# Kernel tuning notes

Hardware: AMD Instinct MI355X
Metric: run time of the kernel (lower is better)

## Reference

```python
import jax, jax.numpy as jnp
import numpy as np

EPS = 1e-6
NUM_HEADS = 16


def _layer_norm(x):
    # LayerNorm32: fp32 layernorm, eps=1e-6, no affine params
    m = jnp.mean(x, axis=-1, keepdims=True)
    v = jnp.var(x, axis=-1, keepdims=True)
    return (x - m) * jax.lax.rsqrt(v + EPS)


def setup_inputs() -> dict:
    key = jax.random.key(0)
    ks = jax.random.split(key, 6)
    B, L, C = 4, 2048, 1024
    H = 4 * C
    s = 0.02
    return {
        "x": jax.random.normal(ks[0], (B, L, C), dtype=jnp.float32),
        "qkv_w": jax.random.normal(ks[1], (C, 3 * C), dtype=jnp.float32) * s,
        "qkv_b": jnp.zeros((3 * C,), dtype=jnp.float32),
        "proj_w": jax.random.normal(ks[2], (C, C), dtype=jnp.float32) * s,
        "proj_b": jnp.zeros((C,), dtype=jnp.float32),
        "fc1_w": jax.random.normal(ks[3], (C, H), dtype=jnp.float32) * s,
        "fc1_b": jnp.zeros((H,), dtype=jnp.float32),
        "fc2_w": jax.random.normal(ks[4], (H, C), dtype=jnp.float32) * s,
        "fc2_b": jnp.zeros((C,), dtype=jnp.float32),
    }


def _block(x, qkv_w, qkv_b, proj_w, proj_b, fc1_w, fc1_b, fc2_w, fc2_b):
    B, L, C = x.shape
    Hn = NUM_HEADS
    D = C // Hn

    # --- attention branch (pre-norm) ---
    h = _layer_norm(x)
    qkv = h @ qkv_w + qkv_b                      # [B, L, 3C]
    qkv = qkv.reshape(B, L, 3, Hn, D)
    q, k, v = qkv[:, :, 0], qkv[:, :, 1], qkv[:, :, 2]  # [B, L, Hn, D]
    scale = 1.0 / jnp.sqrt(jnp.asarray(D, dtype=x.dtype))
    logits = jnp.einsum("bqhd,bkhd->bhqk", q, k) * scale
    attn = jax.nn.softmax(logits, axis=-1)
    o = jnp.einsum("bhqk,bkhd->bqhd", attn, v).reshape(B, L, C)
    o = o @ proj_w + proj_b
    x = x + o

    # --- MLP branch (pre-norm) ---
    h = _layer_norm(x)
    h = jax.nn.gelu(h @ fc1_w + fc1_b, approximate=True)  # tanh GELU
    h = h @ fc2_w + fc2_b
    return x + h


def reference(x, qkv_w, qkv_b, proj_w, proj_b, fc1_w, fc1_b, fc2_w, fc2_b):
    return _block(x, qkv_w, qkv_b, proj_w, proj_b, fc1_w, fc1_b, fc2_w, fc2_b)
```

## Files before the change

kernel.cpp:

```cpp
#include <hip/hip_runtime.h>
#include <hip/hip_bf16.h>

typedef float f32x4 __attribute__((ext_vector_type(4)));
typedef __bf16 bf16x8 __attribute__((ext_vector_type(8)));
typedef unsigned short us8 __attribute__((ext_vector_type(8)));

#define MBYTE (1ull << 20)

#define QSCALE_LOG2E 0.18033688011112042f
#define GELU_K 2.3022081902f

__device__ __forceinline__ unsigned short f2bf(float f) {
    __bf16 h = (__bf16)f;
    return __builtin_bit_cast(unsigned short, h);
}

__device__ __forceinline__ float fast_exp2(float x) {
    return __builtin_amdgcn_exp2f(x);
}

__device__ __forceinline__ f32x4 mfma16(bf16x8 a, bf16x8 b, f32x4 c) {
    return __builtin_amdgcn_mfma_f32_16x16x32_bf16(a, b, c, 0, 0, 0);
}

__device__ __forceinline__ void gload16(const void* g, void* l) {
    __builtin_amdgcn_global_load_lds(
        (const __attribute__((address_space(1))) unsigned int*)g,
        (__attribute__((address_space(3))) unsigned int*)l, 16, 0, 0);
}

__global__ __launch_bounds__(256) void ln_kernel(const float* __restrict__ x,
                                                 unsigned short* __restrict__ out) {
    int row = blockIdx.x;
    int t = threadIdx.x;
    const float* xr = x + (size_t)row * 1024;
    float4 v = *(const float4*)(xr + t * 4);
    float s = v.x + v.y + v.z + v.w;
    float ss = v.x * v.x + v.y * v.y + v.z * v.z + v.w * v.w;
    #pragma unroll
    for (int off = 1; off < 64; off <<= 1) {
        s += __shfl_xor(s, off);
        ss += __shfl_xor(ss, off);
    }
    __shared__ float ps[4], pss[4];
    int wid = t >> 6, lane = t & 63;
    if (lane == 0) { ps[wid] = s; pss[wid] = ss; }
    __syncthreads();
    s = ps[0] + ps[1] + ps[2] + ps[3];
    ss = pss[0] + pss[1] + pss[2] + pss[3];
    float mean = s * (1.0f / 1024.0f);
    float var = ss * (1.0f / 1024.0f) - mean * mean;
    float rs = rsqrtf(var + 1e-6f);
    ushort4 ov;
    ov.x = f2bf((v.x - mean) * rs);
    ov.y = f2bf((v.y - mean) * rs);
    ov.z = f2bf((v.z - mean) * rs);
    ov.w = f2bf((v.w - mean) * rs);
    *(ushort4*)(out + (size_t)row * 1024 + t * 4) = ov;
}

__global__ __launch_bounds__(256) void convT_kernel(const float* __restrict__ W,
                                                    unsigned short* __restrict__ Wt,
                                                    int K, int N) {
    __shared__ float tile[32][33];
    int t = threadIdx.x;
    int tx = t & 31, ty = t >> 5;
    int bx = blockIdx.x, by = blockIdx.y;
    #pragma unroll
    for (int r = 0; r < 4; r++) {
        int row = by * 32 + ty + r * 8;
        int col = bx * 32 + tx;
        tile[ty + r * 8][tx] = W[(size_t)row * N + col];
    }
    __syncthreads();
    #pragma unroll
    for (int r = 0; r < 4; r++) {
        int orow = bx * 32 + ty + r * 8;
        int ocol = by * 32 + tx;
        Wt[(size_t)orow * K + ocol] = f2bf(tile[tx][ty + r * 8]);
    }
}

__global__ __launch_bounds__(256) void vT_kernel(const unsigned short* __restrict__ qkv,
                                                 unsigned short* __restrict__ vT) {
    __shared__ unsigned short tile[32][34];
    int t = threadIdx.x;
    int tx = t & 31, ty = t >> 5;
    int lt = blockIdx.x, dt = blockIdx.y, bh = blockIdx.z;
    int b = bh >> 4, h = bh & 15;
    const unsigned short* src = qkv + (size_t)(b * 2048 + lt * 32) * 3072 + 2048 + h * 64 + dt * 32;
    #pragma unroll
    for (int r = 0; r < 4; r++)
        tile[ty + r * 8][tx] = src[(size_t)(ty + r * 8) * 3072 + tx];
    __syncthreads();
    int perm = (lt & 1) * 32 + ((tx >> 2) & 3) * 8 + ((tx >> 4) & 1) * 4 + (tx & 3);
    unsigned short* dst = vT + ((size_t)bh * 64 + dt * 32) * 2048 + (size_t)(lt >> 1) * 64;
    #pragma unroll
    for (int r = 0; r < 4; r++)
        dst[(size_t)(ty + r * 8) * 2048 + perm] = tile[tx][ty + r * 8];
}

template <int EPI>
__global__ __launch_bounds__(256) void gemm_bt(const unsigned short* __restrict__ A,
                                               const unsigned short* __restrict__ Bt,
                                               const float* __restrict__ bias,
                                               const float* __restrict__ res,
                                               float* __restrict__ outF,
                                               unsigned short* __restrict__ outB,
                                               int M, int N, int K) {
    __shared__ __align__(16) unsigned short As[2][128 * 32];
    __shared__ __align__(16) unsigned short Bs[2][128 * 32];
    int t = threadIdx.x;
    int lane = t & 63, wid = t >> 6;

    int gx = gridDim.x;
    int nwg = gx * gridDim.y;
    int orig = blockIdx.y * gx + blockIdx.x;
    int cpx = nwg >> 3;
    int swz = (orig & 7) * cpx + (orig >> 3);
    int bm = swz / gx, bn = swz % gx;

    int wm = wid >> 1, wn = wid & 1;
    f32x4 acc[4][4] = {};

    int sub = lane >> 2;
    int schunk = ((lane & 3) ^ ((lane >> 3) & 3)) * 8;
    const unsigned short* gA0 = A + (size_t)(bm * 128 + wid * 32 + sub) * K + schunk;
    const unsigned short* gA1 = gA0 + (size_t)16 * K;
    const unsigned short* gB0 = Bt + (size_t)(bn * 128 + wid * 32 + sub) * K + schunk;
    const unsigned short* gB1 = gB0 + (size_t)16 * K;

    int ql = lane & 15;
    int rchunk = (((lane >> 4) ^ ((lane >> 1) & 3))) * 8;

    const int NT = K >> 5;
    gload16(gA0, &As[0][(wid * 32) * 32]);
    gload16(gA1, &As[0][(wid * 32 + 16) * 32]);
    gload16(gB0, &Bs[0][(wid * 32) * 32]);
    gload16(gB1, &Bs[0][(wid * 32 + 16) * 32]);
    __syncthreads();

    int cur = 0;
    for (int tt = 0; tt < NT; ++tt) {
        if (tt + 1 < NT) {
            int k0 = (tt + 1) << 5;
            int nb = cur ^ 1;
            gload16(gA0 + k0, &As[nb][(wid * 32) * 32]);
            gload16(gA1 + k0, &As[nb][(wid * 32 + 16) * 32]);
            gload16(gB0 + k0, &Bs[nb][(wid * 32) * 32]);
            gload16(gB1 + k0, &Bs[nb][(wid * 32 + 16) * 32]);
        }
        bf16x8 af[4], bfr[4];
        #pragma unroll
        for (int m = 0; m < 4; m++)
            af[m] = *(const bf16x8*)&As[cur][(wm * 64 + m * 16 + ql) * 32 + rchunk];
        #pragma unroll
        for (int n = 0; n < 4; n++)
            bfr[n] = *(const bf16x8*)&Bs[cur][(wn * 64 + n * 16 + ql) * 32 + rchunk];
        __builtin_amdgcn_s_setprio(1);
        #pragma unroll
        for (int m = 0; m < 4; m++)
            #pragma unroll
            for (int n = 0; n < 4; n++)
                acc[m][n] = mfma16(af[m], bfr[n], acc[m][n]);
        __builtin_amdgcn_s_setprio(0);
        __syncthreads();
        cur ^= 1;
    }

    #pragma unroll
    for (int m = 0; m < 4; m++) {
        #pragma unroll
        for (int n = 0; n < 4; n++) {
            int col = bn * 128 + wn * 64 + n * 16 + ql;
            float bv = bias[col];
            #pragma unroll
            for (int r = 0; r < 4; r++) {
                int row = bm * 128 + wm * 64 + m * 16 + (lane >> 4) * 4 + r;
                float val = acc[m][n][r] + bv;
                if (EPI == 0) {
                    if (col < 1024) val *= QSCALE_LOG2E;
                    outB[(size_t)row * N + col] = f2bf(val);
                } else if (EPI == 1) {
                    float w = val + 0.044715f * val * val * val;
                    float g = val / (1.0f + fast_exp2(-GELU_K * w));
                    outB[(size_t)row * N + col] = f2bf(g);
                } else {
                    outF[(size_t)row * N + col] = val + res[(size_t)row * N + col];
                }
            }
        }
    }
}

__global__ __launch_bounds__(256) void attn_kernel(const unsigned short* __restrict__ qkv,
                                                   const unsigned short* __restrict__ vT,
                                                   unsigned short* __restrict__ o) {
    int bid = blockIdx.x;
    int qb = bid & 31;
    int bh = bid >> 5;
    int b = bh >> 4, h = bh & 15;
    int t = threadIdx.x, lane = t & 63, wid = t >> 6;

    const unsigned short* base = qkv + (size_t)b * 2048 * 3072 + h * 64;
    const unsigned short* vbase = vT + (size_t)bh * 64 * 2048;

    __shared__ __align__(16) unsigned short Ks[2][64][32];
    __shared__ __align__(16) unsigned short Vs[2][64][32];

    int ql = lane & 15;
    int hi = lane >> 4;

    bf16x8 qf[2];
    {
        int qrow = qb * 64 + wid * 16 + ql;
        const unsigned short* qp = base + (size_t)qrow * 3072 + hi * 8;
        qf[0] = *(const bf16x8*)(qp);
        qf[1] = *(const bf16x8*)(qp + 32);
    }

    float m_r = -1e30f, lpart = 0.0f;
    f32x4 accO[4] = {};

    int srow = wid * 16 + (lane >> 2);
    int schunk = ((lane & 3) ^ ((lane >> 3) & 3)) * 8;
    const unsigned short* gk = base + 1024 + (size_t)srow * 3072 + schunk;
    const unsigned short* gv = vbase + (size_t)srow * 2048 + schunk;
    unsigned short* lK0 = &Ks[0][wid * 16][0];
    unsigned short* lK1 = &Ks[1][wid * 16][0];
    unsigned short* lV0 = &Vs[0][wid * 16][0];
    unsigned short* lV1 = &Vs[1][wid * 16][0];

    int rchunk = (hi ^ ((ql >> 1) & 3)) * 8;

    for (int kt = 0; kt < 32; kt++) {
        __syncthreads();
        gload16(gk, lK0);
        gload16(gk + 32, lK1);
        gload16(gv, lV0);
        gload16(gv + 32, lV1);
        gk += (size_t)64 * 3072;
        gv += 64;
        __syncthreads();

        f32x4 s0 = {}, s1 = {}, s2 = {}, s3 = {};
        #pragma unroll
        for (int c = 0; c < 2; c++) {
            bf16x8 a0 = *(const bf16x8*)&Ks[c][ 0 + ql][rchunk];
            bf16x8 a1 = *(const bf16x8*)&Ks[c][16 + ql][rchunk];
            bf16x8 a2 = *(const bf16x8*)&Ks[c][32 + ql][rchunk];
            bf16x8 a3 = *(const bf16x8*)&Ks[c][48 + ql][rchunk];
            s0 = mfma16(a0, qf[c], s0);
            s1 = mfma16(a1, qf[c], s1);
            s2 = mfma16(a2, qf[c], s2);
            s3 = mfma16(a3, qf[c], s3);
        }

        float mx = fmaxf(fmaxf(fmaxf(s0[0], s0[1]), fmaxf(s0[2], s0[3])),
                         fmaxf(fmaxf(s1[0], s1[1]), fmaxf(s1[2], s1[3])));
        mx = fmaxf(mx, fmaxf(fmaxf(s2[0], s2[1]), fmaxf(s2[2], s2[3])));
        mx = fmaxf(mx, fmaxf(fmaxf(s3[0], s3[1]), fmaxf(s3[2], s3[3])));
        if (!__all(mx <= m_r + 8.0f)) {
            float mm = fmaxf(mx, __shfl_xor(mx, 16));
            mm = fmaxf(mm, __shfl_xor(mm, 32));
            float mnew = fmaxf(m_r, mm);
            float corr = fast_exp2(m_r - mnew);
            m_r = mnew;
            lpart *= corr;
            #pragma unroll
            for (int r = 0; r < 4; r++) {
                float cq = __shfl(corr, hi * 4 + r);
                accO[0][r] *= cq; accO[1][r] *= cq;
                accO[2][r] *= cq; accO[3][r] *= cq;
            }
        }

        us8 pu0, pu1;
        #pragma unroll
        for (int j = 0; j < 4; j++) {
            float pa = fast_exp2(s0[j] - m_r);
            float pb = fast_exp2(s1[j] - m_r);
            float pc = fast_exp2(s2[j] - m_r);
            float pd = fast_exp2(s3[j] - m_r);
            lpart += (pa + pb) + (pc + pd);
            pu0[j] = f2bf(pa); pu0[4 + j] = f2bf(pb);
            pu1[j] = f2bf(pc); pu1[4 + j] = f2bf(pd);
        }
        bf16x8 paf0 = __builtin_bit_cast(bf16x8, pu0);
        bf16x8 paf1 = __builtin_bit_cast(bf16x8, pu1);

        #pragma unroll
        for (int nn = 0; nn < 4; nn++) {
            bf16x8 bv0 = *(const bf16x8*)&Vs[0][nn * 16 + ql][rchunk];
            bf16x8 bv1 = *(const bf16x8*)&Vs[1][nn * 16 + ql][rchunk];
            accO[nn] = mfma16(paf0, bv0, accO[nn]);
            accO[nn] = mfma16(paf1, bv1, accO[nn]);
        }
    }

    lpart += __shfl_xor(lpart, 16);
    lpart += __shfl_xor(lpart, 32);
    float rinv = 1.0f / lpart;
    #pragma unroll
    for (int r = 0; r < 4; r++) {
        float rq = __shfl(rinv, hi * 4 + r);
        int row = qb * 64 + wid * 16 + hi * 4 + r;
        #pragma unroll
        for (int nn = 0; nn < 4; nn++) {
            int col = h * 64 + nn * 16 + ql;
            o[(size_t)(b * 2048 + row) * 1024 + col] = f2bf(accO[nn][r] * rq);
        }
    }
}

extern "C" void kernel_launch(void* const* d_in, const int* in_sizes, int n_in,
                              void* d_out, int out_size, void* d_ws, size_t ws_size,
                              hipStream_t stream) {
    const float* x      = (const float*)d_in[0];
    const float* qkv_w  = (const float*)d_in[1];
    const float* qkv_b  = (const float*)d_in[2];
    const float* proj_w = (const float*)d_in[3];
    const float* proj_b = (const float*)d_in[4];
    const float* fc1_w  = (const float*)d_in[5];
    const float* fc1_b  = (const float*)d_in[6];
    const float* fc2_w  = (const float*)d_in[7];
    const float* fc2_b  = (const float*)d_in[8];
    float* out = (float*)d_out;

    char* ws = (char*)d_ws;
    unsigned short* h_buf   = (unsigned short*)(ws + 0 * MBYTE);
    unsigned short* qkv_buf = (unsigned short*)(ws + 16 * MBYTE);
    unsigned short* o_buf   = (unsigned short*)(ws + 64 * MBYTE);
    float*          x2_buf  = (float*)(ws + 80 * MBYTE);
    unsigned short* vT_buf  = (unsigned short*)(ws + 80 * MBYTE);
    unsigned short* wqT     = (unsigned short*)(ws + 112 * MBYTE);
    unsigned short* wpT     = (unsigned short*)(ws + 118 * MBYTE);
    unsigned short* w1T     = (unsigned short*)(ws + 120 * MBYTE);
    unsigned short* w2T     = (unsigned short*)(ws + 128 * MBYTE);
    unsigned short* g_buf   = (unsigned short*)(ws + 16 * MBYTE);

    const int M = 8192;

    convT_kernel<<<dim3(3072 / 32, 1024 / 32), 256, 0, stream>>>(qkv_w, wqT, 1024, 3072);
    convT_kernel<<<dim3(1024 / 32, 1024 / 32), 256, 0, stream>>>(proj_w, wpT, 1024, 1024);
    convT_kernel<<<dim3(4096 / 32, 1024 / 32), 256, 0, stream>>>(fc1_w, w1T, 1024, 4096);
    convT_kernel<<<dim3(1024 / 32, 4096 / 32), 256, 0, stream>>>(fc2_w, w2T, 4096, 1024);

    ln_kernel<<<M, 256, 0, stream>>>(x, h_buf);

    gemm_bt<0><<<dim3(3072 / 128, M / 128), 256, 0, stream>>>(
        h_buf, wqT, qkv_b, nullptr, nullptr, qkv_buf, M, 3072, 1024);

    vT_kernel<<<dim3(64, 2, 64), 256, 0, stream>>>(qkv_buf, vT_buf);

    attn_kernel<<<dim3(32 * 64), 256, 0, stream>>>(qkv_buf, vT_buf, o_buf);

    gemm_bt<2><<<dim3(1024 / 128, M / 128), 256, 0, stream>>>(
        o_buf, wpT, proj_b, x, x2_buf, nullptr, M, 1024, 1024);

    ln_kernel<<<M, 256, 0, stream>>>(x2_buf, h_buf);

    gemm_bt<1><<<dim3(4096 / 128, M / 128), 256, 0, stream>>>(
        h_buf, w1T, fc1_b, nullptr, nullptr, g_buf, M, 4096, 1024);

    gemm_bt<2><<<dim3(1024 / 128, M / 128), 256, 0, stream>>>(
        g_buf, w2T, fc2_b, x2_buf, out, nullptr, M, 1024, 4096);
}
```

Before: 448.7 us.

## Triple-buffer LDS tiles in GEMM and attention with vmcnt-based waits

Both the bf16 GEMM and the attention kernel now use three LDS stages and prefetch the tile two iterations ahead. Each iteration waits only on the oldest outstanding global-to-LDS loads (s_waitcnt vmcnt(4)) and then issues a single barrier. Previously the attention kernel loaded each K/V tile and waited on it synchronously. The aim is to hide global memory latency behind MFMA work. In exchange LDS use per block grows, which may lower occupancy, and correctness now depends on the hand-counted vmcnt values matching how the compiler orders the loads.

```diff
diff --git a/kernel.cpp b/kernel.cpp
--- a/kernel.cpp
+++ b/kernel.cpp
@@ -108,8 +108,8 @@
                                                float* __restrict__ outF,
                                                unsigned short* __restrict__ outB,
                                                int M, int N, int K) {
-    __shared__ __align__(16) unsigned short As[2][128 * 32];
-    __shared__ __align__(16) unsigned short Bs[2][128 * 32];
+    __shared__ __align__(16) unsigned short As[3][128 * 32];
+    __shared__ __align__(16) unsigned short Bs[3][128 * 32];
     int t = threadIdx.x;
     int lane = t & 63, wid = t >> 6;
 
@@ -134,29 +134,35 @@
     int rchunk = (((lane >> 4) ^ ((lane >> 1) & 3))) * 8;
 
     const int NT = K >> 5;
-    gload16(gA0, &As[0][(wid * 32) * 32]);
-    gload16(gA1, &As[0][(wid * 32 + 16) * 32]);
-    gload16(gB0, &Bs[0][(wid * 32) * 32]);
-    gload16(gB1, &Bs[0][(wid * 32 + 16) * 32]);
-    __syncthreads();
+
+    auto STAGE = [&](int buf, int tile) {
+        int k0 = tile << 5;
+        gload16(gA0 + k0, &As[buf][(wid * 32) * 32]);
+        gload16(gA1 + k0, &As[buf][(wid * 32 + 16) * 32]);
+        gload16(gB0 + k0, &Bs[buf][(wid * 32) * 32]);
+        gload16(gB1 + k0, &Bs[buf][(wid * 32 + 16) * 32]);
+    };
+
+    STAGE(0, 0);
+    STAGE(1, 1);
+    asm volatile("s_waitcnt vmcnt(4)" ::: "memory");
+    __builtin_amdgcn_s_barrier();
 
     int cur = 0;
     for (int tt = 0; tt < NT; ++tt) {
-        if (tt + 1 < NT) {
-            int k0 = (tt + 1) << 5;
-            int nb = cur ^ 1;
-            gload16(gA0 + k0, &As[nb][(wid * 32) * 32]);
-            gload16(gA1 + k0, &As[nb][(wid * 32 + 16) * 32]);
-            gload16(gB0 + k0, &Bs[nb][(wid * 32) * 32]);
-            gload16(gB1 + k0, &Bs[nb][(wid * 32 + 16) * 32]);
-        }
+        int pre = cur + 2; if (pre >= 3) pre -= 3;
+        bool do_stage = (tt + 2 < NT);
+        if (do_stage) STAGE(pre, tt + 2);
+
+        const unsigned short* curA = &As[cur][0];
+        const unsigned short* curB = &Bs[cur][0];
         bf16x8 af[4], bfr[4];
         #pragma unroll
         for (int m = 0; m < 4; m++)
-            af[m] = *(const bf16x8*)&As[cur][(wm * 64 + m * 16 + ql) * 32 + rchunk];
+            af[m] = *(const bf16x8*)&curA[(wm * 64 + m * 16 + ql) * 32 + rchunk];
         #pragma unroll
         for (int n = 0; n < 4; n++)
-            bfr[n] = *(const bf16x8*)&Bs[cur][(wn * 64 + n * 16 + ql) * 32 + rchunk];
+            bfr[n] = *(const bf16x8*)&curB[(wn * 64 + n * 16 + ql) * 32 + rchunk];
         __builtin_amdgcn_s_setprio(1);
         #pragma unroll
         for (int m = 0; m < 4; m++)
@@ -164,8 +170,12 @@
             for (int n = 0; n < 4; n++)
                 acc[m][n] = mfma16(af[m], bfr[n], acc[m][n]);
         __builtin_amdgcn_s_setprio(0);
-        __syncthreads();
-        cur ^= 1;
+
+        if (do_stage) asm volatile("s_waitcnt vmcnt(4)" ::: "memory");
+        else          asm volatile("s_waitcnt vmcnt(0)" ::: "memory");
+        __builtin_amdgcn_sched_barrier(0);
+        __builtin_amdgcn_s_barrier();
+        cur = (cur == 2) ? 0 : cur + 1;
     }
 
     #pragma unroll
@@ -205,8 +215,8 @@
     const unsigned short* base = qkv + (size_t)b * 2048 * 3072 + h * 64;
     const unsigned short* vbase = vT + (size_t)bh * 64 * 2048;
 
-    __shared__ __align__(16) unsigned short Ks[2][64][32];
-    __shared__ __align__(16) unsigned short Vs[2][64][32];
+    __shared__ __align__(16) unsigned short Ks[3][2][64][32];
+    __shared__ __align__(16) unsigned short Vs[3][2][64][32];
 
     int ql = lane & 15;
     int hi = lane >> 4;
@@ -226,30 +236,40 @@
     int schunk = ((lane & 3) ^ ((lane >> 3) & 3)) * 8;
     const unsigned short* gk = base + 1024 + (size_t)srow * 3072 + schunk;
     const unsigned short* gv = vbase + (size_t)srow * 2048 + schunk;
-    unsigned short* lK0 = &Ks[0][wid * 16][0];
-    unsigned short* lK1 = &Ks[1][wid * 16][0];
-    unsigned short* lV0 = &Vs[0][wid * 16][0];
-    unsigned short* lV1 = &Vs[1][wid * 16][0];
 
     int rchunk = (hi ^ ((ql >> 1) & 3)) * 8;
 
+    auto STAGE = [&](int buf, const unsigned short* pk, const unsigned short* pv) {
+        gload16(pk, &Ks[buf][0][wid * 16][0]);
+        gload16(pk + 32, &Ks[buf][1][wid * 16][0]);
+        gload16(pv, &Vs[buf][0][wid * 16][0]);
+        gload16(pv + 32, &Vs[buf][1][wid * 16][0]);
+    };
+
+    const size_t KSTRIDE = (size_t)64 * 3072;
+
+    STAGE(0, gk, gv);
+    STAGE(1, gk + KSTRIDE, gv + 64);
+    gk += 2 * KSTRIDE; gv += 128;
+    asm volatile("s_waitcnt vmcnt(4)" ::: "memory");
+    __builtin_amdgcn_s_barrier();
+
+    int cur = 0;
     for (int kt = 0; kt < 32; kt++) {
-        __syncthreads();
-        gload16(gk, lK0);
-        gload16(gk + 32, lK1);
-        gload16(gv, lV0);
-        gload16(gv + 32, lV1);
-        gk += (size_t)64 * 3072;
-        gv += 64;
-        __syncthreads();
+        int pre = cur + 2; if (pre >= 3) pre -= 3;
+        bool do_stage = (kt < 30);
+        if (do_stage) {
+            STAGE(pre, gk, gv);
+            gk += KSTRIDE; gv += 64;
+        }
 
         f32x4 s0 = {}, s1 = {}, s2 = {}, s3 = {};
         #pragma unroll
         for (int c = 0; c < 2; c++) {
-            bf16x8 a0 = *(const bf16x8*)&Ks[c][ 0 + ql][rchunk];
-            bf16x8 a1 = *(const bf16x8*)&Ks[c][16 + ql][rchunk];
-            bf16x8 a2 = *(const bf16x8*)&Ks[c][32 + ql][rchunk];
-            bf16x8 a3 = *(const bf16x8*)&Ks[c][48 + ql][rchunk];
+            bf16x8 a0 = *(const bf16x8*)&Ks[cur][c][ 0 + ql][rchunk];
+            bf16x8 a1 = *(const bf16x8*)&Ks[cur][c][16 + ql][rchunk];
+            bf16x8 a2 = *(const bf16x8*)&Ks[cur][c][32 + ql][rchunk];
+            bf16x8 a3 = *(const bf16x8*)&Ks[cur][c][48 + ql][rchunk];
             s0 = mfma16(a0, qf[c], s0);
             s1 = mfma16(a1, qf[c], s1);
             s2 = mfma16(a2, qf[c], s2);
@@ -291,11 +311,17 @@
 
         #pragma unroll
         for (int nn = 0; nn < 4; nn++) {
-            bf16x8 bv0 = *(const bf16x8*)&Vs[0][nn * 16 + ql][rchunk];
-            bf16x8 bv1 = *(const bf16x8*)&Vs[1][nn * 16 + ql][rchunk];
+            bf16x8 bv0 = *(const bf16x8*)&Vs[cur][0][nn * 16 + ql][rchunk];
+            bf16x8 bv1 = *(const bf16x8*)&Vs[cur][1][nn * 16 + ql][rchunk];
             accO[nn] = mfma16(paf0, bv0, accO[nn]);
             accO[nn] = mfma16(paf1, bv1, accO[nn]);
         }
+
+        if (do_stage) asm volatile("s_waitcnt vmcnt(4)" ::: "memory");
+        else          asm volatile("s_waitcnt vmcnt(0)" ::: "memory");
+        __builtin_amdgcn_sched_barrier(0);
+        __builtin_amdgcn_s_barrier();
+        cur = (cur == 2) ? 0 : cur + 1;
     }
 
     lpart += __shfl_xor(lpart, 16);
```

After: 459.3 us. 1.02x slower.

## Replace GEMM with 8-wave 256-row tile kernel and split-K pipelined staging

Applied to the files above, without the earlier changes.

Swaps the 128x128, 4-wave bf16 GEMM for an 8-wave kernel with 256-row tiles (256x128, or 256x256 for fc1). The K step is 64, split into two 32-wide halves, and global loads for the next tile are interleaved between MFMA phases using explicit vmcnt waits and raw barriers. The goal is more operand reuse per LDS load and better overlap of memory traffic with MFMA work. The cost is much more LDS and more accumulator registers (up to 8x4 f32x4 per lane), which may cut occupancy. There are also fewer workgroups for the N=1024 GEMMs (256 per launch), which may underfill the 256 CUs.

```diff
diff --git a/kernel.cpp b/kernel.cpp
--- a/kernel.cpp
+++ b/kernel.cpp
@@ -100,18 +100,24 @@
         dst[(size_t)(ty + r * 8) * 2048 + perm] = tile[tx][ty + r * 8];
 }
 
-template <int EPI>
-__global__ __launch_bounds__(256) void gemm_bt(const unsigned short* __restrict__ A,
-                                               const unsigned short* __restrict__ Bt,
-                                               const float* __restrict__ bias,
-                                               const float* __restrict__ res,
-                                               float* __restrict__ outF,
-                                               unsigned short* __restrict__ outB,
-                                               int M, int N, int K) {
-    __shared__ __align__(16) unsigned short As[2][128 * 32];
-    __shared__ __align__(16) unsigned short Bs[2][128 * 32];
+template <int EPI, int BN>
+__global__ __launch_bounds__(512) void gemm8(const unsigned short* __restrict__ A,
+                                             const unsigned short* __restrict__ Bt,
+                                             const float* __restrict__ bias,
+                                             const float* __restrict__ res,
+                                             float* __restrict__ outF,
+                                             unsigned short* __restrict__ outB,
+                                             int M, int N, int K) {
+    constexpr int WCOLS = (BN == 256) ? 64 : 32;
+    constexpr int NREP = WCOLS / 16;
+    constexpr int NH = NREP / 2;
+
+    __shared__ __align__(16) unsigned short As[2][2][256 * 32];
+    __shared__ __align__(16) unsigned short Bs[2][2][BN * 32];
+
     int t = threadIdx.x;
     int lane = t & 63, wid = t >> 6;
+    int ql = lane & 15, hi = lane >> 4;
 
     int gx = gridDim.x;
     int nwg = gx * gridDim.y;
@@ -120,63 +126,100 @@
     int swz = (orig & 7) * cpx + (orig >> 3);
     int bm = swz / gx, bn = swz % gx;
 
-    int wm = wid >> 1, wn = wid & 1;
-    f32x4 acc[4][4] = {};
-
-    int sub = lane >> 2;
+    int wm = wid >> 2, wn = wid & 3;
+
+    f32x4 acc[8][NREP] = {};
+
+    int srow = wid * 16 + (lane >> 2);
     int schunk = ((lane & 3) ^ ((lane >> 3) & 3)) * 8;
-    const unsigned short* gA0 = A + (size_t)(bm * 128 + wid * 32 + sub) * K + schunk;
-    const unsigned short* gA1 = gA0 + (size_t)16 * K;
-    const unsigned short* gB0 = Bt + (size_t)(bn * 128 + wid * 32 + sub) * K + schunk;
-    const unsigned short* gB1 = gB0 + (size_t)16 * K;
-
-    int ql = lane & 15;
-    int rchunk = (((lane >> 4) ^ ((lane >> 1) & 3))) * 8;
-
-    const int NT = K >> 5;
-    gload16(gA0, &As[0][(wid * 32) * 32]);
-    gload16(gA1, &As[0][(wid * 32 + 16) * 32]);
-    gload16(gB0, &Bs[0][(wid * 32) * 32]);
-    gload16(gB1, &Bs[0][(wid * 32 + 16) * 32]);
-    __syncthreads();
-
-    int cur = 0;
-    for (int tt = 0; tt < NT; ++tt) {
-        if (tt + 1 < NT) {
-            int k0 = (tt + 1) << 5;
-            int nb = cur ^ 1;
-            gload16(gA0 + k0, &As[nb][(wid * 32) * 32]);
-            gload16(gA1 + k0, &As[nb][(wid * 32 + 16) * 32]);
-            gload16(gB0 + k0, &Bs[nb][(wid * 32) * 32]);
-            gload16(gB1 + k0, &Bs[nb][(wid * 32 + 16) * 32]);
-        }
-        bf16x8 af[4], bfr[4];
-        #pragma unroll
-        for (int m = 0; m < 4; m++)
-            af[m] = *(const bf16x8*)&As[cur][(wm * 64 + m * 16 + ql) * 32 + rchunk];
-        #pragma unroll
-        for (int n = 0; n < 4; n++)
-            bfr[n] = *(const bf16x8*)&Bs[cur][(wn * 64 + n * 16 + ql) * 32 + rchunk];
+    const unsigned short* gA = A + (size_t)(bm * 256 + srow) * K + schunk;
+    const unsigned short* gB = Bt + (size_t)(bn * BN + srow) * K + schunk;
+
+    int rch = (hi ^ ((ql >> 1) & 3)) * 8;
+
+    auto STAGE_A = [&](int q, int kh, int kt) {
+        size_t off = (size_t)kt * 64 + kh * 32;
+        gload16(gA + off, &As[q][kh][(wid * 16) * 32]);
+        gload16(gA + (size_t)128 * K + off, &As[q][kh][(128 + wid * 16) * 32]);
+    };
+    auto STAGE_B = [&](int q, int kh, int kt) {
+        size_t off = (size_t)kt * 64 + kh * 32;
+        gload16(gB + off, &Bs[q][kh][(wid * 16) * 32]);
+        if constexpr (BN == 256)
+            gload16(gB + (size_t)128 * K + off, &Bs[q][kh][(128 + wid * 16) * 32]);
+    };
+
+    bf16x8 af[8];
+    auto READ_A = [&](int p, int kh) {
+        #pragma unroll
+        for (int m = 0; m < 8; m++)
+            af[m] = *(const bf16x8*)&As[p][kh][(wm * 128 + m * 16 + ql) * 32 + rch];
+    };
+    auto MFMA_PH = [&](int p, int kh, int nh) {
+        bf16x8 bf0[NH];
+        #pragma unroll
+        for (int j = 0; j < NH; j++)
+            bf0[j] = *(const bf16x8*)&Bs[p][kh][(wn * WCOLS + (nh * NH + j) * 16 + ql) * 32 + rch];
         __builtin_amdgcn_s_setprio(1);
         #pragma unroll
-        for (int m = 0; m < 4; m++)
+        for (int m = 0; m < 8; m++)
             #pragma unroll
-            for (int n = 0; n < 4; n++)
-                acc[m][n] = mfma16(af[m], bfr[n], acc[m][n]);
+            for (int j = 0; j < NH; j++)
+                acc[m][nh * NH + j] = mfma16(af[m], bf0[j], acc[m][nh * NH + j]);
         __builtin_amdgcn_s_setprio(0);
-        __syncthreads();
-        cur ^= 1;
-    }
-
-    #pragma unroll
-    for (int m = 0; m < 4; m++) {
-        #pragma unroll
-        for (int n = 0; n < 4; n++) {
-            int col = bn * 128 + wn * 64 + n * 16 + ql;
+    };
+
+    const int NT = K >> 6;
+
+    STAGE_A(0, 0, 0); STAGE_B(0, 0, 0); STAGE_A(0, 1, 0); STAGE_B(0, 1, 0);
+    asm volatile("s_waitcnt vmcnt(0)" ::: "memory");
+    __builtin_amdgcn_s_barrier();
+    __builtin_amdgcn_sched_barrier(0);
+
+    int p = 0;
+    for (int kt = 0; kt < NT; ++kt) {
+        int q = p ^ 1;
+        bool st = (kt + 1 < NT);
+        if (st) STAGE_A(q, 0, kt + 1);
+        READ_A(p, 0);
+        MFMA_PH(p, 0, 0);
+        if (st) STAGE_B(q, 0, kt + 1);
+        MFMA_PH(p, 0, 1);
+        if (st) {
+            if constexpr (BN == 256) asm volatile("s_waitcnt vmcnt(4)" ::: "memory");
+            else                     asm volatile("s_waitcnt vmcnt(3)" ::: "memory");
+        } else {
+            asm volatile("s_waitcnt vmcnt(0)" ::: "memory");
+        }
+        __builtin_amdgcn_sched_barrier(0);
+        __builtin_amdgcn_s_barrier();
+        __builtin_amdgcn_sched_barrier(0);
+        if (st) STAGE_A(q, 1, kt + 1);
+        READ_A(p, 1);
+        MFMA_PH(p, 1, 0);
+        if (st) STAGE_B(q, 1, kt + 1);
+        MFMA_PH(p, 1, 1);
+        if (st) {
+            if constexpr (BN == 256) asm volatile("s_waitcnt vmcnt(4)" ::: "memory");
+            else                     asm volatile("s_waitcnt vmcnt(3)" ::: "memory");
+        } else {
+            asm volatile("s_waitcnt vmcnt(0)" ::: "memory");
+        }
+        __builtin_amdgcn_sched_barrier(0);
+        __builtin_amdgcn_s_barrier();
+        __builtin_amdgcn_sched_barrier(0);
+        p ^= 1;
+    }
+
+    #pragma unroll
+    for (int m = 0; m < 8; m++) {
+        #pragma unroll
+        for (int n = 0; n < NREP; n++) {
+            int col = bn * BN + wn * WCOLS + n * 16 + ql;
             float bv = bias[col];
             #pragma unroll
             for (int r = 0; r < 4; r++) {
-                int row = bm * 128 + wm * 64 + m * 16 + (lane >> 4) * 4 + r;
+                int row = bm * 256 + wm * 128 + m * 16 + hi * 4 + r;
                 float val = acc[m][n][r] + bv;
                 if (EPI == 0) {
                     if (col < 1024) val *= QSCALE_LOG2E;
@@ -348,21 +391,21 @@
 
     ln_kernel<<<M, 256, 0, stream>>>(x, h_buf);
 
-    gemm_bt<0><<<dim3(3072 / 128, M / 128), 256, 0, stream>>>(
+    gemm8<0, 128><<<dim3(3072 / 128, M / 256), 512, 0, stream>>>(
         h_buf, wqT, qkv_b, nullptr, nullptr, qkv_buf, M, 3072, 1024);
 
     vT_kernel<<<dim3(64, 2, 64), 256, 0, stream>>>(qkv_buf, vT_buf);
 
     attn_kernel<<<dim3(32 * 64), 256, 0, stream>>>(qkv_buf, vT_buf, o_buf);
 
-    gemm_bt<2><<<dim3(1024 / 128, M / 128), 256, 0, stream>>>(
+    gemm8<2, 128><<<dim3(1024 / 128, M / 256), 512, 0, stream>>>(
         o_buf, wpT, proj_b, x, x2_buf, nullptr, M, 1024, 1024);
 
     ln_kernel<<<M, 256, 0, stream>>>(x2_buf, h_buf);
 
-    gemm_bt<1><<<dim3(4096 / 128, M / 128), 256, 0, stream>>>(
+    gemm8<1, 256><<<dim3(4096 / 256, M / 256), 512, 0, stream>>>(
         h_buf, w1T, fc1_b, nullptr, nullptr, g_buf, M, 4096, 1024);
 
-    gemm_bt<2><<<dim3(1024 / 128, M / 128), 256, 0, stream>>>(
+    gemm8<2, 128><<<dim3(1024 / 128, M / 256), 512, 0, stream>>>(
         g_buf, w2T, fc2_b, x2_buf, out, nullptr, M, 1024, 4096);
 }
```

Result: slower. 499.6 us (+11.4%).

## Rewrite GEMM as 256x128 tile, 8-wave, 3-stage pipelined kernel with BK=64

Applied to the files above, without the earlier changes.

Replaces the double-buffered 128x128 BK=32 GEMM with a 512-thread kernel computing 256x128 tiles, BK=64 and a triple-buffered LDS ring. Global loads for A and B are issued two k-steps ahead and interleaved with the MFMA phases. Explicit vmcnt waits plus a raw s_barrier replace __syncthreads. The aim is to hide global latency better and raise the MFMA-to-load ratio per k-step. In exchange it uses much more LDS (144KB), which limits occupancy, and it relies on correct hand-counted vmcnt values.

```diff
diff --git a/kernel.cpp b/kernel.cpp
--- a/kernel.cpp
+++ b/kernel.cpp
@@ -101,17 +101,19 @@
 }
 
 template <int EPI>
-__global__ __launch_bounds__(256) void gemm_bt(const unsigned short* __restrict__ A,
-                                               const unsigned short* __restrict__ Bt,
-                                               const float* __restrict__ bias,
-                                               const float* __restrict__ res,
-                                               float* __restrict__ outF,
-                                               unsigned short* __restrict__ outB,
-                                               int M, int N, int K) {
-    __shared__ __align__(16) unsigned short As[2][128 * 32];
-    __shared__ __align__(16) unsigned short Bs[2][128 * 32];
+__global__ __launch_bounds__(512) void gemm3s(const unsigned short* __restrict__ A,
+                                              const unsigned short* __restrict__ Bt,
+                                              const float* __restrict__ bias,
+                                              const float* __restrict__ res,
+                                              float* __restrict__ outF,
+                                              unsigned short* __restrict__ outB,
+                                              int M, int N, int K) {
+    __shared__ __align__(16) unsigned short As[3][256 * 64];
+    __shared__ __align__(16) unsigned short Bs[3][128 * 64];
+
     int t = threadIdx.x;
     int lane = t & 63, wid = t >> 6;
+    int ql = lane & 15, hi = lane >> 4;
 
     int gx = gridDim.x;
     int nwg = gx * gridDim.y;
@@ -123,49 +125,83 @@
     int wm = wid >> 1, wn = wid & 1;
     f32x4 acc[4][4] = {};
 
-    int sub = lane >> 2;
-    int schunk = ((lane & 3) ^ ((lane >> 3) & 3)) * 8;
-    const unsigned short* gA0 = A + (size_t)(bm * 128 + wid * 32 + sub) * K + schunk;
-    const unsigned short* gA1 = gA0 + (size_t)16 * K;
-    const unsigned short* gB0 = Bt + (size_t)(bn * 128 + wid * 32 + sub) * K + schunk;
-    const unsigned short* gB1 = gB0 + (size_t)16 * K;
-
-    int ql = lane & 15;
-    int rchunk = (((lane >> 4) ^ ((lane >> 1) & 3))) * 8;
-
-    const int NT = K >> 5;
-    gload16(gA0, &As[0][(wid * 32) * 32]);
-    gload16(gA1, &As[0][(wid * 32 + 16) * 32]);
-    gload16(gB0, &Bs[0][(wid * 32) * 32]);
-    gload16(gB1, &Bs[0][(wid * 32 + 16) * 32]);
-    __syncthreads();
-
-    int cur = 0;
-    for (int tt = 0; tt < NT; ++tt) {
-        if (tt + 1 < NT) {
-            int k0 = (tt + 1) << 5;
-            int nb = cur ^ 1;
-            gload16(gA0 + k0, &As[nb][(wid * 32) * 32]);
-            gload16(gA1 + k0, &As[nb][(wid * 32 + 16) * 32]);
-            gload16(gB0 + k0, &Bs[nb][(wid * 32) * 32]);
-            gload16(gB1 + k0, &Bs[nb][(wid * 32 + 16) * 32]);
-        }
-        bf16x8 af[4], bfr[4];
-        #pragma unroll
-        for (int m = 0; m < 4; m++)
-            af[m] = *(const bf16x8*)&As[cur][(wm * 64 + m * 16 + ql) * 32 + rchunk];
-        #pragma unroll
-        for (int n = 0; n < 4; n++)
-            bfr[n] = *(const bf16x8*)&Bs[cur][(wn * 64 + n * 16 + ql) * 32 + rchunk];
+    int lrow = lane >> 3;
+    int schunk = ((lane & 7) ^ lrow) * 8;
+    const unsigned short* gA = A + (size_t)(bm * 256 + wid * 8 + lrow) * K + schunk;
+    const unsigned short* gB = Bt + (size_t)(bn * 128 + wid * 8 + lrow) * K + schunk;
+
+    auto STAGE_A = [&](int buf, int kt) {
+        size_t ko = (size_t)kt * 64;
+        #pragma unroll
+        for (int rd = 0; rd < 4; rd++)
+            gload16(gA + (size_t)rd * 64 * K + ko, &As[buf][(rd * 64 + wid * 8) * 64]);
+    };
+    auto STAGE_B = [&](int buf, int kt) {
+        size_t ko = (size_t)kt * 64;
+        #pragma unroll
+        for (int rd = 0; rd < 2; rd++)
+            gload16(gB + (size_t)rd * 64 * K + ko, &Bs[buf][(rd * 64 + wid * 8) * 64]);
+    };
+
+    int rsl0 = ((0 + hi) ^ (ql & 7)) * 8;
+    int rsl1 = ((4 + hi) ^ (ql & 7)) * 8;
+
+    const int NT = K >> 6;
+
+    STAGE_A(0, 0); STAGE_B(0, 0);
+    STAGE_A(1, 1); STAGE_B(1, 1);
+    asm volatile("s_waitcnt vmcnt(6)" ::: "memory");
+    __builtin_amdgcn_sched_barrier(0);
+    __builtin_amdgcn_s_barrier();
+
+    int p = 0;
+    for (int kt = 0; kt < NT; ++kt) {
+        int q = p + 2; if (q >= 3) q -= 3;
+        bool st = (kt + 2 < NT);
+
+        if (st) STAGE_A(q, kt + 2);
+        bf16x8 af0[4], af1[4], bf0[2], bf1[2];
+        #pragma unroll
+        for (int m = 0; m < 4; m++) {
+            af0[m] = *(const bf16x8*)&As[p][(wm * 64 + m * 16 + ql) * 64 + rsl0];
+            af1[m] = *(const bf16x8*)&As[p][(wm * 64 + m * 16 + ql) * 64 + rsl1];
+        }
+        #pragma unroll
+        for (int n = 0; n < 2; n++) {
+            bf0[n] = *(const bf16x8*)&Bs[p][(wn * 64 + n * 16 + ql) * 64 + rsl0];
+            bf1[n] = *(const bf16x8*)&Bs[p][(wn * 64 + n * 16 + ql) * 64 + rsl1];
+        }
         __builtin_amdgcn_s_setprio(1);
         #pragma unroll
         for (int m = 0; m < 4; m++)
             #pragma unroll
-            for (int n = 0; n < 4; n++)
-                acc[m][n] = mfma16(af[m], bfr[n], acc[m][n]);
+            for (int n = 0; n < 2; n++) {
+                acc[m][n] = mfma16(af0[m], bf0[n], acc[m][n]);
+                acc[m][n] = mfma16(af1[m], bf1[n], acc[m][n]);
+            }
         __builtin_amdgcn_s_setprio(0);
-        __syncthreads();
-        cur ^= 1;
+
+        if (st) STAGE_B(q, kt + 2);
+        #pragma unroll
+        for (int n = 0; n < 2; n++) {
+            bf0[n] = *(const bf16x8*)&Bs[p][(wn * 64 + (2 + n) * 16 + ql) * 64 + rsl0];
+            bf1[n] = *(const bf16x8*)&Bs[p][(wn * 64 + (2 + n) * 16 + ql) * 64 + rsl1];
+        }
+        __builtin_amdgcn_s_setprio(1);
+        #pragma unroll
+        for (int m = 0; m < 4; m++)
+            #pragma unroll
+            for (int n = 0; n < 2; n++) {
+                acc[m][2 + n] = mfma16(af0[m], bf0[n], acc[m][2 + n]);
+                acc[m][2 + n] = mfma16(af1[m], bf1[n], acc[m][2 + n]);
+            }
+        __builtin_amdgcn_s_setprio(0);
+
+        if (st) asm volatile("s_waitcnt vmcnt(6)" ::: "memory");
+        else    asm volatile("s_waitcnt vmcnt(0)" ::: "memory");
+        __builtin_amdgcn_sched_barrier(0);
+        __builtin_amdgcn_s_barrier();
+        p += 1; if (p == 3) p = 0;
     }
 
     #pragma unroll
@@ -176,7 +212,7 @@
             float bv = bias[col];
             #pragma unroll
             for (int r = 0; r < 4; r++) {
-                int row = bm * 128 + wm * 64 + m * 16 + (lane >> 4) * 4 + r;
+                int row = bm * 256 + wm * 64 + m * 16 + hi * 4 + r;
                 float val = acc[m][n][r] + bv;
                 if (EPI == 0) {
                     if (col < 1024) val *= QSCALE_LOG2E;
@@ -348,21 +384,21 @@
 
     ln_kernel<<<M, 256, 0, stream>>>(x, h_buf);
 
-    gemm_bt<0><<<dim3(3072 / 128, M / 128), 256, 0, stream>>>(
+    gemm3s<0><<<dim3(3072 / 128, M / 256), 512, 0, stream>>>(
         h_buf, wqT, qkv_b, nullptr, nullptr, qkv_buf, M, 3072, 1024);
 
     vT_kernel<<<dim3(64, 2, 64), 256, 0, stream>>>(qkv_buf, vT_buf);
 
     attn_kernel<<<dim3(32 * 64), 256, 0, stream>>>(qkv_buf, vT_buf, o_buf);
 
-    gemm_bt<2><<<dim3(1024 / 128, M / 128), 256, 0, stream>>>(
+    gemm3s<2><<<dim3(1024 / 128, M / 256), 512, 0, stream>>>(
         o_buf, wpT, proj_b, x, x2_buf, nullptr, M, 1024, 1024);
 
     ln_kernel<<<M, 256, 0, stream>>>(x2_buf, h_buf);
 
-    gemm_bt<1><<<dim3(4096 / 128, M / 128), 256, 0, stream>>>(
+    gemm3s<1><<<dim3(4096 / 128, M / 256), 512, 0, stream>>>(
         h_buf, w1T, fc1_b, nullptr, nullptr, g_buf, M, 4096, 1024);
 
-    gemm_bt<2><<<dim3(1024 / 128, M / 128), 256, 0, stream>>>(
+    gemm3s<2><<<dim3(1024 / 128, M / 256), 512, 0, stream>>>(
         g_buf, w2T, fc2_b, x2_buf, out, nullptr, M, 1024, 4096);
 }
```

After: 485.1 us. +8.1%, slower.
